# Kernel tuning notes

Measured on AMD Instinct MI355X. Metric: run time of the kernel, lower is better.

The kernel has to match this reference:

```python
import jax, jax.numpy as jnp
import numpy as np

B = 4          # batch of packed sequences
Q_LEN = 8192   # QPos.size
K_LEN = 8192   # KPos.size
N_SEG = 8      # packed segments per row
WINDOW = 1024  # sliding window
OFFSET = 0     # causal offset


def setup_inputs() -> dict:
    key = jax.random.key(0)
    k_seg, k_exp = jax.random.split(key, 2)
    # sorted segment ids mimic sequence packing (contiguous segments)
    q_seg = jnp.sort(jax.random.randint(k_seg, (B, Q_LEN), 0, N_SEG), axis=-1).astype(jnp.int32)
    kv_seg = q_seg  # self-attention: same packing for q and kv
    # explicit mask: mostly-allowed boolean mask (e.g. padding/document mask)
    explicit = jax.random.bernoulli(k_exp, 0.9, (Q_LEN, K_LEN))
    return {
        "explicit_mask": explicit,
        "q_segment_ids": q_seg,
        "kv_segment_ids": kv_seg,
        "q_len": Q_LEN,
        "k_len": K_LEN,
        "causal_offset": OFFSET,
        "window": WINDOW,
    }


def reference(explicit_mask, q_segment_ids, kv_segment_ids, q_len, k_len, causal_offset, window):
    """Faithful translation of AttentionMask.materialize (full q/k slices).

    mask = causal & explicit & sliding_window & segment, conjunction via
    combine_masks_and. Returns bool [B, Q, K].
    """
    q_pos = jnp.arange(q_len, dtype=jnp.int32)[:, None]   # [Q, 1]
    k_pos = jnp.arange(k_len, dtype=jnp.int32)[None, :]   # [1, K]
    diff = q_pos - k_pos                                   # [Q, K]
    # causal with offset: q_pos >= k_pos - offset  (offset future tokens visible)
    causal = diff >= -causal_offset
    # causal sliding window: 0 <= q_pos - k_pos < window
    sw = (diff >= 0) & (diff < window)
    mask2d = causal & explicit_mask & sw                   # [Q, K]
    # segment mask: q_seg[b, q] == kv_seg[b, k]
    seg = q_segment_ids[:, :, None] == kv_segment_ids[:, None, :]  # [B, Q, K]
    return mask2d[None, :, :] & seg
```

## Files before the change

### kernel.cpp

```cpp
#include <hip/hip_runtime.h>

#define QL 8192
#define KL 8192
#define BB 4
#define K4 (KL / 4)

__global__ __launch_bounds__(256) void mask_kernel(
    const int* __restrict__ expl,
    const int* __restrict__ qseg,
    const int* __restrict__ kseg,
    const int* __restrict__ p_off,
    const int* __restrict__ p_win,
    int* __restrict__ out)
{
    const int offset = *p_off;
    const int window = *p_win;

    const long long i = (long long)blockIdx.x * 256 + threadIdx.x;
    const int k4 = (int)(i & (K4 - 1));
    const long long qb = i >> 11;
    const int q = (int)(qb & (QL - 1));
    const int b = (int)(qb >> 13);
    const int k0 = k4 << 2;

    const int dmin = (-offset > 0) ? -offset : 0;
    const int lo = q - (window - 1);
    const int hi = q - dmin;

    int4 v = make_int4(0, 0, 0, 0);

    if (k0 <= hi && (k0 + 3) >= lo) {
        const int qs = qseg[b * QL + q];
        const int4 e = *reinterpret_cast<const int4*>(expl + (long long)q * KL + k0);
        const int4 s = *reinterpret_cast<const int4*>(kseg + b * KL + k0);
        int k = k0;
        v.x = (k >= lo && k <= hi && e.x != 0 && s.x == qs) ? 1 : 0; ++k;
        v.y = (k >= lo && k <= hi && e.y != 0 && s.y == qs) ? 1 : 0; ++k;
        v.z = (k >= lo && k <= hi && e.z != 0 && s.z == qs) ? 1 : 0; ++k;
        v.w = (k >= lo && k <= hi && e.w != 0 && s.w == qs) ? 1 : 0;
    }

    reinterpret_cast<int4*>(out)[i] = v;
}

extern "C" void kernel_launch(void* const* d_in, const int* in_sizes, int n_in,
                              void* d_out, int out_size, void* d_ws, size_t ws_size,
                              hipStream_t stream) {
    const int* expl  = (const int*)d_in[0];
    const int* qseg  = (const int*)d_in[1];
    const int* kseg  = (const int*)d_in[2];
    const int* p_off = (const int*)d_in[5];
    const int* p_win = (const int*)d_in[6];
    int* out = (int*)d_out;

    const long long total_i4 = (long long)BB * QL * K4;
    const int block = 256;
    const long long grid = total_i4 / block;

    mask_kernel<<<dim3((unsigned)grid), dim3(block), 0, stream>>>(
        expl, qseg, kseg, p_off, p_win, out);
}
```

Before: 1.156 ms.

## Assign one row per block and use nontemporal vector stores

Each block now covers one full (batch, query) row, and every thread walks 8 strided int4 chunks, replacing one thread per int4 over a very large grid. Per-row values (segment id, window bounds, row pointers) are computed once per block, and output writes use nontemporal stores so the 1 GiB int32 mask output streams past the cache. The cost is fewer threads in flight per block, though 32K blocks still fill the device easily.

```diff
diff --git a/kernel.cpp b/kernel.cpp
--- a/kernel.cpp
+++ b/kernel.cpp
@@ -4,6 +4,9 @@
 #define KL 8192
 #define BB 4
 #define K4 (KL / 4)
+#define CHUNKS 8
+
+typedef int v4i __attribute__((ext_vector_type(4)));
 
 __global__ __launch_bounds__(256) void mask_kernel(
     const int* __restrict__ expl,
@@ -13,34 +16,41 @@
     const int* __restrict__ p_win,
     int* __restrict__ out)
 {
+    const int row = blockIdx.x;
+    const int q   = row & (QL - 1);
+    const int b   = row >> 13;
+
     const int offset = *p_off;
     const int window = *p_win;
-
-    const long long i = (long long)blockIdx.x * 256 + threadIdx.x;
-    const int k4 = (int)(i & (K4 - 1));
-    const long long qb = i >> 11;
-    const int q = (int)(qb & (QL - 1));
-    const int b = (int)(qb >> 13);
-    const int k0 = k4 << 2;
 
     const int dmin = (-offset > 0) ? -offset : 0;
     const int lo = q - (window - 1);
     const int hi = q - dmin;
 
-    int4 v = make_int4(0, 0, 0, 0);
+    const int qs = qseg[row];
 
-    if (k0 <= hi && (k0 + 3) >= lo) {
-        const int qs = qseg[b * QL + q];
-        const int4 e = *reinterpret_cast<const int4*>(expl + (long long)q * KL + k0);
-        const int4 s = *reinterpret_cast<const int4*>(kseg + b * KL + k0);
-        int k = k0;
-        v.x = (k >= lo && k <= hi && e.x != 0 && s.x == qs) ? 1 : 0; ++k;
-        v.y = (k >= lo && k <= hi && e.y != 0 && s.y == qs) ? 1 : 0; ++k;
-        v.z = (k >= lo && k <= hi && e.z != 0 && s.z == qs) ? 1 : 0; ++k;
-        v.w = (k >= lo && k <= hi && e.w != 0 && s.w == qs) ? 1 : 0;
+    const v4i* __restrict__ erow = reinterpret_cast<const v4i*>(expl) + (long long)q * K4;
+    const v4i* __restrict__ srow = reinterpret_cast<const v4i*>(kseg) + (long long)b * K4;
+    v4i* __restrict__ orow       = reinterpret_cast<v4i*>(out)        + (long long)row * K4;
+
+    const int t = threadIdx.x;
+
+#pragma unroll
+    for (int j = 0; j < CHUNKS; ++j) {
+        const int k4 = j * 256 + t;
+        const int k0 = k4 << 2;
+        v4i v = (v4i){0, 0, 0, 0};
+        if (k0 <= hi && (k0 + 3) >= lo) {
+            const v4i e = erow[k4];
+            const v4i s = srow[k4];
+            int k = k0;
+            v.x = (k >= lo && k <= hi && e.x != 0 && s.x == qs) ? 1 : 0; ++k;
+            v.y = (k >= lo && k <= hi && e.y != 0 && s.y == qs) ? 1 : 0; ++k;
+            v.z = (k >= lo && k <= hi && e.z != 0 && s.z == qs) ? 1 : 0; ++k;
+            v.w = (k >= lo && k <= hi && e.w != 0 && s.w == qs) ? 1 : 0;
+        }
+        __builtin_nontemporal_store(v, orow + k4);
     }
-
-    reinterpret_cast<int4*>(out)[i] = v;
 }
 
 extern "C" void kernel_launch(void* const* d_in, const int* in_sizes, int n_in,
@@ -53,10 +63,7 @@
     const int* p_win = (const int*)d_in[6];
     int* out = (int*)d_out;
 
-    const long long total_i4 = (long long)BB * QL * K4;
-    const int block = 256;
-    const long long grid = total_i4 / block;
-
-    mask_kernel<<<dim3((unsigned)grid), dim3(block), 0, stream>>>(
+    const int grid = BB * QL;
+    mask_kernel<<<dim3(grid), dim3(256), 0, stream>>>(
         expl, qseg, kseg, p_off, p_win, out);
 }
```

Result: no change. 1.166 ms (+0.9%).
